# Kernel optimization log

Hardware: AMD Instinct MI355X
Metric: run time of the kernel (lower is better)

Reference implementation:

```python
import jax, jax.numpy as jnp
import numpy as np
from jax import lax

B = 8
SEQ_LEN = 336
PRED_LEN = 336
D_MODEL = 32
D_FF = 64
TOP_K = 3
NUM_KERNELS = 6
WAVELET_SCALE = 4
PERIOD_COEFF = 0.5
T_TOTAL = SEQ_LEN + PRED_LEN
KMAX = 2 * NUM_KERNELS - 1  # 11, largest Inception kernel
N_WAVELET_SCALES = 8


def _int_psi_morlet():
    # pywt integrate_wavelet('morl', precision=10)
    xg = np.linspace(-8.0, 8.0, 1 << 10)
    psi = np.exp(-xg ** 2 / 2.0) * np.cos(5.0 * xg)
    step = xg[1] - xg[0]
    return np.cumsum(psi) * step, xg


def cwt_morl(data, scales):
    # data: (B, N, T) -> coeffs (S, B, N, T); follows pywt/ptwt cwt(..., 'morl')
    int_psi, xg = _int_psi_morlet()
    step = xg[1] - xg[0]
    b, n, t = data.shape
    flat = data.reshape(-1, t)
    outs = []
    for s in scales:
        j = (np.arange(s * (xg[-1] - xg[0]) + 1) / (s * step)).astype(np.int64)
        j = j[j < int_psi.size]
        filt = jnp.asarray(int_psi[j][::-1].copy(), dtype=data.dtype)
        conv = jax.vmap(lambda r: jnp.convolve(r, filt, mode='full'))(flat)
        coef = (-float(np.sqrt(s))) * jnp.diff(conv, axis=-1)
        d = (coef.shape[-1] - t) / 2.0
        coef = coef[:, int(np.floor(d)): coef.shape[-1] - int(np.ceil(d))]
        outs.append(coef.reshape(b, n, t))
    return jnp.stack(outs, 0)


def _conv2d_same(x, w, bias, pad_h, pad_w):
    y = lax.conv_general_dilated(x, w, (1, 1), [(pad_h, pad_h), (pad_w, pad_w)],
                                 dimension_numbers=('NCHW', 'OIHW', 'NCHW'))
    return y + bias[None, :, None, None]


def _inception(x, w, bias):
    # w: (K, O, I, 11, 11) with each k-th kernel (size 2k+1) zero-padded to 11x11.
    # mean of K 'same' convs == one conv with the mean kernel (conv is linear).
    return _conv2d_same(x, w.mean(0), bias.mean(0), KMAX // 2, KMAX // 2)


def _period_conv(x, w1, b1, w2, b2):
    h = jax.nn.gelu(_inception(x, w1, b1), approximate=False)
    return _inception(h, w2, b2)


def _dct2(x):
    # DCT-II over last dim, norm=None (matches torch helper: 2 * Re(W * FFT(perm(x))))
    n = x.shape[-1]
    v = jnp.concatenate([x[..., ::2], x[..., 1::2][..., ::-1]], axis=-1)
    vc = jnp.fft.fft(v, axis=-1)
    k = -jnp.arange(n, dtype=x.dtype) * (np.pi / (2 * n))
    return 2.0 * (vc.real * jnp.cos(k) - vc.imag * jnp.sin(k))


def _dct_block(xcl, ln_w, ln_b, w_fc1, w_fc2):
    # xcl: (B, C, L). Per-channel DCT loop in torch == DCT over last dim.
    f = _dct2(xcl)
    mu = f.mean(-1, keepdims=True)
    var = ((f - mu) ** 2).mean(-1, keepdims=True)
    ln = (f - mu) / jnp.sqrt(var + 1e-6) * ln_w + ln_b
    h = jax.nn.relu(jnp.einsum('bcl,dc->bdl', ln, w_fc1))  # 1x1 conv1d, no bias
    lr = jax.nn.sigmoid(jnp.einsum('bdl,cd->bcl', h, w_fc2))
    return xcl * lr


def _top_periods(x):
    # torch.topk on batch/channel-averaged rfft magnitude; indices are detached
    amp = np.abs(np.fft.rfft(np.asarray(jax.device_get(x)), axis=1))
    freq = amp.mean(axis=(0, 2))
    freq[0] = 0.0
    return np.argsort(-freq)[:TOP_K]


def _forward(x, w_inc1, b_inc1, w_inc2, b_inc2, w_scale, b_scale,
             ln_w, ln_b, w_fc1, w_fc2, w_proj, b_proj, top_list):
    b, t, n = x.shape
    amp = jnp.abs(jnp.fft.rfft(x, axis=1))          # (B, F, N)
    period_weight = amp.mean(-1)[:, top_list]       # (B, k)

    res = []
    for idx in top_list:
        p = t // int(idx)
        length = t if t % p == 0 else (t // p + 1) * p
        out = x if length == t else jnp.concatenate(
            [x, jnp.zeros((b, length - t, n), x.dtype)], axis=1)
        out = out.reshape(b, length // p, p, n).transpose(0, 3, 1, 2)  # (B,N,L/p,p)
        out = _period_conv(out, w_inc1, b_inc1, w_inc2, b_inc2)
        out = out.transpose(0, 2, 3, 1).reshape(b, length, n)[:, :t, :]
        res.append(out)
    res = jnp.stack(res, -1)                         # (B,T,N,k)
    pw = jax.nn.softmax(period_weight, axis=1)       # (B,k)

    scales = 2.0 ** np.linspace(-1, WAVELET_SCALE, N_WAVELET_SCALES)
    coeffs = cwt_morl(x.transpose(0, 2, 1), scales).transpose(1, 2, 0, 3)  # (B,N,8,T)
    wr = _period_conv(coeffs, w_inc1, b_inc1, w_inc2, b_inc2)              # (B,N,8,T)
    # depthwise Conv2d(kernel=(8,1), groups=d_model), squeezes scale axis
    wr = jnp.einsum('bcst,cs->bct', wr, w_scale) + b_scale[None, :, None]  # (B,N,T)
    wr = wr.transpose(0, 2, 1)                       # (B,T,N)

    pc10 = PERIOD_COEFF ** 10
    out = (1.0 - pc10) * wr + pc10 * jnp.einsum('btnk,bk->btn', res, pw)
    out = out + x
    xc = _dct_block(out.transpose(0, 2, 1), ln_w, ln_b, w_fc1, w_fc2)
    out = xc.transpose(0, 2, 1) + x
    y = jnp.einsum('bnt,pt->bnp', out.transpose(0, 2, 1), w_proj) + b_proj
    return y.transpose(0, 2, 1)                      # (B, PRED_LEN, N)


def _masked_inception_weight(key, out_c, in_c):
    w = jax.random.normal(key, (NUM_KERNELS, out_c, in_c, KMAX, KMAX), jnp.float32) * 0.05
    mask = np.zeros((NUM_KERNELS, 1, 1, KMAX, KMAX), np.float32)
    for i in range(NUM_KERNELS):
        ks = 2 * i + 1
        lo = (KMAX - ks) // 2
        mask[i, 0, 0, lo:lo + ks, lo:lo + ks] = 1.0
    return w * jnp.asarray(mask)


def setup_inputs() -> dict:
    key = jax.random.key(0)
    ks = jax.random.split(key, 12)
    return {
        'x': jax.random.normal(ks[0], (B, T_TOTAL, D_MODEL), jnp.float32),
        'w_inc1': _masked_inception_weight(ks[1], D_FF, D_MODEL),
        'b_inc1': jax.random.normal(ks[2], (NUM_KERNELS, D_FF), jnp.float32) * 0.02,
        'w_inc2': _masked_inception_weight(ks[3], D_MODEL, D_FF),
        'b_inc2': jax.random.normal(ks[4], (NUM_KERNELS, D_MODEL), jnp.float32) * 0.02,
        'w_scale': jax.random.normal(ks[5], (D_MODEL, 8), jnp.float32) * 0.1,
        'b_scale': jax.random.normal(ks[6], (D_MODEL,), jnp.float32) * 0.02,
        'ln_w': jnp.ones((T_TOTAL,), jnp.float32),
        'ln_b': jnp.zeros((T_TOTAL,), jnp.float32),
        'w_fc1': jax.random.normal(ks[7], (2 * D_MODEL, D_MODEL), jnp.float32) * 0.1,
        'w_fc2': jax.random.normal(ks[8], (D_MODEL, 2 * D_MODEL), jnp.float32) * 0.1,
        'w_proj': jax.random.normal(ks[9], (PRED_LEN, T_TOTAL), jnp.float32) * 0.02,
        'b_proj': jax.random.normal(ks[10], (PRED_LEN,), jnp.float32) * 0.02,
    }


def reference(x, w_inc1, b_inc1, w_inc2, b_inc2, w_scale, b_scale,
              ln_w, ln_b, w_fc1, w_fc2, w_proj, b_proj):
    top_list = _top_periods(x)  # concrete (detached) indices, like torch
    return _forward(x, w_inc1, b_inc1, w_inc2, b_inc2, w_scale, b_scale,
                    ln_w, ln_b, w_fc1, w_fc2, w_proj, b_proj, top_list)
```

## Files before the change

kernel.cpp:

```cpp
#include <hip/hip_runtime.h>
#include <math.h>

#ifndef M_PI
#define M_PI 3.14159265358979323846
#endif

typedef __attribute__((ext_vector_type(8))) short bf16x8;
typedef __attribute__((ext_vector_type(4))) float f32x4;

struct CwtP {
  double sstep[8];
  float  sqs[8];
  int    L[8];
  int    st0[8];
};

#define OFF_DTABC 0
#define OFF_DTABS 5376
#define OFF_AMP   10752
#define OFF_DCT   32320
#define OFF_DFILT 43072
#define OFF_PW    51520
#define OFF_META  51616
#define OFF_B1    51712
#define OFF_B2    51968
#define OFF_W1T   52224
#define OFF_W2T   547840
#define OFF_XT    1043456
#define OFF_PADW  1731584
#define OFF_PADW2 8016896
#define OFF_WRC2  20587520
#define OFF_POUT2 26092544
#define OFF_OUT1T 30221312
#define OFF_PADP  OFF_PADW
#define OFF_PADP2 OFF_PADW2
#define OFF_LN    26092544
#define OFF_HB    26780672
#define OFF_OUT2T 28156928

__device__ inline unsigned short f2b(float f) {
  unsigned int u = __float_as_uint(f);
  unsigned int r = (u + 0x7fffu + ((u >> 16) & 1u)) >> 16;
  return (unsigned short)r;
}

__global__ void k_tables(double* __restrict__ dtabc, double* __restrict__ dtabs,
                         float* __restrict__ dcttab) {
  int tid = threadIdx.x;
  for (int j = tid; j < 672; j += blockDim.x) {
    double a = (2.0 * M_PI * (double)j) / 672.0;
    dtabc[j] = cos(a);
    dtabs[j] = sin(a);
  }
  for (int j = tid; j < 2688; j += blockDim.x) {
    dcttab[j] = (float)cos(M_PI * (double)j / 1344.0);
  }
}

__global__ void k_wmeanb(const float* __restrict__ w1, const float* __restrict__ b1,
                         const float* __restrict__ w2, const float* __restrict__ b2,
                         unsigned short* __restrict__ W1T, unsigned short* __restrict__ W2T,
                         float* __restrict__ B1, float* __restrict__ B2) {
  int i = blockIdx.x * blockDim.x + threadIdx.x;
  const float inv6 = 1.0f / 6.0f;
  if (i < 247808) {
    float s1 = 0.f, s2 = 0.f;
#pragma unroll
    for (int g = 0; g < 6; ++g) { s1 += w1[g * 247808 + i]; s2 += w2[g * 247808 + i]; }
    s1 *= inv6; s2 *= inv6;
    {
      int co = i / 3872; int r = i - co * 3872;
      int ci = r / 121;  int tap = r - ci * 121;
      W1T[tap * 2048 + co * 32 + ci] = f2b(s1);
    }
    {
      int co = i / 7744; int r = i - co * 7744;
      int ci = r / 121;  int tap = r - ci * 121;
      W2T[tap * 2048 + co * 64 + ci] = f2b(s2);
    }
  } else {
    int j = i - 247808;
    if (j < 64) {
      float s = 0.f;
#pragma unroll
      for (int g = 0; g < 6; ++g) s += b1[g * 64 + j];
      B1[j] = s * inv6;
    } else if (j < 96) {
      int c = j - 64;
      float s = 0.f;
#pragma unroll
      for (int g = 0; g < 6; ++g) s += b2[g * 32 + c];
      B2[c] = s * inv6;
    }
  }
}

__global__ void k_xT(const float* __restrict__ x, float* __restrict__ xT) {
  int i = blockIdx.x * 256 + threadIdx.x;
  if (i >= 8 * 672 * 32) return;
  int n = i & 31;
  int t = (i >> 5) % 672;
  int b = i / (32 * 672);
  xT[(b * 32 + n) * 672 + t] = x[i];
}

__global__ void k_dft(const float* __restrict__ x, const double* __restrict__ tc,
                      const double* __restrict__ ts, double* __restrict__ amp) {
  int k = blockIdx.x, b = blockIdx.y;
  int tid = threadIdx.x;
  int n = tid & 31, half = tid >> 5;
  double re = 0.0, im = 0.0;
  for (int t = half; t < 672; t += 2) {
    double xv = (double)x[(b * 672 + t) * 32 + n];
    int idx = (k * t) % 672;
    re += xv * tc[idx];
    im += xv * ts[idx];
  }
  re += __shfl_xor(re, 32);
  im += __shfl_xor(im, 32);
  double a = sqrt(re * re + im * im);
  for (int off = 16; off >= 1; off >>= 1) a += __shfl_xor(a, off);
  if (tid == 0) amp[b * 337 + k] = a * (1.0 / 32.0);
}

__global__ void k_top(const double* __restrict__ amp, int* __restrict__ meta,
                      float* __restrict__ pw) {
  __shared__ double fr[337];
  __shared__ int sidx[3];
  int tid = threadIdx.x;
  for (int k = tid; k < 337; k += 64) {
    double s = 0.0;
    for (int b = 0; b < 8; ++b) s += amp[b * 337 + k];
    fr[k] = (k == 0) ? -1.0 : s * 0.125;
  }
  __syncthreads();
  if (tid == 0) {
    for (int r = 0; r < 3; ++r) {
      int best = 1; double bv = fr[1];
      for (int k = 2; k < 337; ++k) if (fr[k] > bv) { bv = fr[k]; best = k; }
      fr[best] = -2.0;
      sidx[r] = best;
      meta[r] = best;
      int p = 672 / best;
      meta[3 + r] = p;
      int len = (672 % p == 0) ? 672 : (672 / p + 1) * p;
      meta[6 + r] = len;
      meta[9 + r] = len / p;
    }
  }
  __syncthreads();
  if (tid < 8) {
    int b = tid;
    float v0 = (float)amp[b * 337 + sidx[0]];
    float v1 = (float)amp[b * 337 + sidx[1]];
    float v2 = (float)amp[b * 337 + sidx[2]];
    float m = fmaxf(v0, fmaxf(v1, v2));
    float e0 = expf(v0 - m), e1 = expf(v1 - m), e2 = expf(v2 - m);
    float inv = 1.0f / (e0 + e1 + e2);
    pw[b * 3 + 0] = e0 * inv;
    pw[b * 3 + 1] = e1 * inv;
    pw[b * 3 + 2] = e2 * inv;
  }
}

__global__ void k_dfilt(float* __restrict__ dfilt, CwtP P) {
  __shared__ double ipsi[1024];
  int tid = threadIdx.x;
  const double step = 16.0 / 1023.0;
  double xg = (tid == 1023) ? 8.0 : (-8.0 + (double)tid * step);
  ipsi[tid] = exp(-0.5 * xg * xg) * cos(5.0 * xg);
  __syncthreads();
  for (int off = 1; off < 1024; off <<= 1) {
    double v = ipsi[tid];
    double a = (tid >= off) ? ipsi[tid - off] : 0.0;
    __syncthreads();
    ipsi[tid] = v + a;
    __syncthreads();
  }
  for (int s = 0; s < 8; ++s) {
    int L = P.L[s];
    double sstep = P.sstep[s];
    for (int q = tid; q <= L; q += 1024) {
      float fq = 0.f, fqm = 0.f;
      if (q < L)  { long j = (long)((double)(L - 1 - q) / sstep); fq  = (float)(ipsi[j] * step); }
      if (q >= 1) { long j = (long)((double)(L - q) / sstep);     fqm = (float)(ipsi[j] * step); }
      dfilt[s * 264 + q] = fq - fqm;
    }
  }
}

__global__ void k_cwt(const float* __restrict__ xT, const float* __restrict__ dfilt,
                      unsigned short* __restrict__ PADW, CwtP P) {
  int s = blockIdx.x, n = blockIdx.y, b = blockIdx.z;
  __shared__ float row[672];
  __shared__ float df[264];
  int tid = threadIdx.x;
  int L = P.L[s], st0 = P.st0[s];
  float sq = P.sqs[s];
  for (int i = tid; i < 672; i += blockDim.x) row[i] = xT[(b * 32 + n) * 672 + i];
  for (int i = tid; i <= L; i += blockDim.x) df[i] = dfilt[s * 264 + i];
  __syncthreads();
  for (int t = tid; t < 672; t += blockDim.x) {
    float acc = 0.f;
    int base = t + st0 + 1;
    for (int q = 0; q <= L; ++q) {
      int idx = base - q;
      if (idx >= 0 && idx < 672) acc += df[q] * row[idx];
    }
    PADW[((size_t)(b * 18 + s + 5) * 682 + (t + 5)) * 32 + n] = f2b(-sq * acc);
  }
}

__global__ void k_zero(float4* __restrict__ p, int n16) {
  int i = blockIdx.x * 256 + threadIdx.x;
  int stride = gridDim.x * 256;
  for (; i < n16; i += stride) p[i] = float4{0.f, 0.f, 0.f, 0.f};
}

__global__ void k_pfill(const float* __restrict__ x, unsigned short* __restrict__ PADP,
                        const int* __restrict__ meta, int k) {
  int i = blockIdx.x * 256 + threadIdx.x;
  if (i >= 8 * 672 * 32) return;
  int W = meta[3 + k], H = meta[9 + k];
  int PW = W + 10;
  int ci = i & 31;
  int t = (i >> 5) % 672;
  int b = i / 21504;
  int h = t / W, w = t - h * W;
  PADP[((size_t)(b * (H + 10) + h + 5) * PW + (w + 5)) * 32 + ci] = f2b(x[i]);
}

template <int CIN, int COUT, int MODE>
__global__ __launch_bounds__(256) void k_conv(
    const unsigned short* __restrict__ Pin, const unsigned short* __restrict__ Wt,
    const float* __restrict__ bias, void* __restrict__ outp,
    int Hs, int Ws, int gi, const int* __restrict__ meta, int HWcap, int Tlim) {
  constexpr int NA = COUT / 16;
  constexpr int NS = CIN / 32;
  constexpr int RED = NA * 4 + 1;
  __shared__ float red[4][64][RED];

  int H = Hs, W = Ws;
  if (gi >= 0) { W = meta[3 + gi]; H = meta[9 + gi]; }
  int PW = W + 10;
  int HW = H * W;
  int Tout = (HW < Tlim) ? HW : Tlim;
  int tiles = (Tout + 15) >> 4;
  int total = 8 * tiles;
  int gid = blockIdx.x;
  if (gid >= total) return;
  int q = total >> 3, rr = total & 7;
  int xcd = gid & 7, lid = gid >> 3;
  int wid = (xcd < rr) ? (xcd * (q + 1) + lid)
                       : (rr * (q + 1) + (xcd - rr) * q + lid);
  int ti = wid % tiles; int b = wid / tiles;
  int wv = threadIdx.x >> 6;
  int l = threadIdx.x & 63;
  int lr = l & 15, lk = l >> 4;

  int t = ti * 16 + lr;
  bool valid = (t < Tout);
  unsigned tt = valid ? (unsigned)t : 0u;
  unsigned h = tt / (unsigned)W;
  unsigned w = tt - h * (unsigned)W;

  int h0 = (ti * 16) / W;
  int tl5 = ti * 16 + 15; if (tl5 >= Tout) tl5 = Tout - 1;
  int h1 = tl5 / W;
  int kh_lo = (h1 >= 5) ? 0 : 5 - h1;
  int kh_hi = (H + 4 - h0 < 10) ? (H + 4 - h0) : 10;

  const unsigned short* pB =
      Pin + ((size_t)(b * (H + 10) + h) * PW + w) * CIN + lk * 8;

  f32x4 acc[NA];
#pragma unroll
  for (int c = 0; c < NA; ++c) acc[c] = f32x4{0.f, 0.f, 0.f, 0.f};

  for (int kh = kh_lo + wv; kh <= kh_hi; kh += 4) {
    const unsigned short* pBr = pB + (size_t)kh * PW * CIN;
    const unsigned short* pA =
        Wt + (size_t)(kh * 11) * COUT * CIN + (size_t)lr * CIN + lk * 8;
#pragma unroll
    for (int s = 0; s < NS; ++s) {
      bf16x8 bfr[11];
#pragma unroll
      for (int kw = 0; kw < 11; ++kw)
        bfr[kw] = *(const bf16x8*)(const void*)(pBr + kw * CIN + s * 32);
#pragma unroll
      for (int kw = 0; kw < 11; ++kw) {
#pragma unroll
        for (int c = 0; c < NA; ++c) {
          bf16x8 af = *(const bf16x8*)(const void*)(
              pA + (size_t)kw * COUT * CIN + c * 16 * CIN + s * 32);
          acc[c] = __builtin_amdgcn_mfma_f32_16x16x32_bf16(af, bfr[kw], acc[c], 0, 0, 0);
        }
      }
    }
  }

#pragma unroll
  for (int c = 0; c < NA; ++c)
#pragma unroll
    for (int q2 = 0; q2 < 4; ++q2) red[wv][l][c * 4 + q2] = acc[c][q2];
  __syncthreads();

  if (wv >= NA || !valid) return;
  int c = wv;
  int co0 = c * 16 + lk * 4;
  float v[4];
#pragma unroll
  for (int q2 = 0; q2 < 4; ++q2) {
    float s = red[0][l][c * 4 + q2] + red[1][l][c * 4 + q2] +
              red[2][l][c * 4 + q2] + red[3][l][c * 4 + q2];
    s += bias[co0 + q2];
    if (MODE == 0) s = 0.5f * s * (1.0f + erff(s * 0.70710678118654752f));
    v[q2] = s;
  }
  if (MODE == 0) {
    unsigned short* Po = (unsigned short*)outp;
    size_t oa = ((size_t)(b * (H + 10) + h + 5) * PW + (w + 5)) * COUT + co0;
    uint2 pk;
    pk.x = (unsigned int)f2b(v[0]) | ((unsigned int)f2b(v[1]) << 16);
    pk.y = (unsigned int)f2b(v[2]) | ((unsigned int)f2b(v[3]) << 16);
    *(uint2*)(void*)(Po + oa) = pk;
  } else {
    float* Fo = (float*)outp;
    size_t oa = ((size_t)b * HWcap + t) * COUT + co0;
    f32x4 vv = {v[0], v[1], v[2], v[3]};
    *(f32x4*)(void*)(Fo + oa) = vv;
  }
}

__global__ void k_combine(const float* __restrict__ WRC2, const float* __restrict__ w_scale,
                          const float* __restrict__ b_scale, const float* __restrict__ POUT2,
                          const float* __restrict__ pw, const float* __restrict__ xT,
                          float* __restrict__ out1T) {
  int b = blockIdx.y;
  int tid = threadIdx.x;
  int n = tid & 31;
  int t = blockIdx.x * 8 + (tid >> 5);
  float wv = b_scale[n];
#pragma unroll
  for (int s = 0; s < 8; ++s)
    wv += WRC2[((size_t)(b * 5376 + s * 672 + t)) * 32 + n] * w_scale[n * 8 + s];
  float p0 = pw[b * 3 + 0], p1 = pw[b * 3 + 1], p2 = pw[b * 3 + 2];
  size_t bi = (size_t)(b * 1344 + t) * 32 + n;
  float rs = p0 * POUT2[bi] + p1 * POUT2[344064 + bi] + p2 * POUT2[688128 + bi];
  const float pc10 = 1.0f / 1024.0f;
  out1T[(b * 32 + n) * 672 + t] =
      (1.0f - pc10) * wv + pc10 * rs + xT[(b * 32 + n) * 672 + t];
}

__global__ void k_dct_ln(const float* __restrict__ out1T, const float* __restrict__ dcttab,
                         const float* __restrict__ ln_w, const float* __restrict__ ln_b,
                         float* __restrict__ ln) {
  int c = blockIdx.x, b = blockIdx.y;
  __shared__ float row[672];
  __shared__ float tab[2688];
  __shared__ float s1[4], s2[4];
  int tid = threadIdx.x;
  for (int i = tid; i < 672; i += 256) row[i] = out1T[(b * 32 + c) * 672 + i];
  for (int i = tid; i < 2688; i += 256) tab[i] = dcttab[i];
  __syncthreads();
  float fv[3];
  float sum = 0.f, sumsq = 0.f;
#pragma unroll
  for (int r = 0; r < 3; ++r) {
    int k = tid + r * 256;
    float acc = 0.f;
    if (k < 672) {
      int idx = k;
      int stp = (2 * k) % 2688;
      for (int m = 0; m < 672; ++m) {
        acc += row[m] * tab[idx];
        idx += stp;
        if (idx >= 2688) idx -= 2688;
      }
      acc *= 2.0f;
      sum += acc;
      sumsq += acc * acc;
    }
    fv[r] = acc;
  }
  for (int off = 32; off >= 1; off >>= 1) {
    sum += __shfl_xor(sum, off);
    sumsq += __shfl_xor(sumsq, off);
  }
  if ((tid & 63) == 0) { s1[tid >> 6] = sum; s2[tid >> 6] = sumsq; }
  __syncthreads();
  float tsum = s1[0] + s1[1] + s1[2] + s1[3];
  float tsq = s2[0] + s2[1] + s2[2] + s2[3];
  float mu = tsum * (1.0f / 672.0f);
  float var = tsq * (1.0f / 672.0f) - mu * mu;
  float rstd = rsqrtf(var + 1e-6f);
#pragma unroll
  for (int r = 0; r < 3; ++r) {
    int k = tid + r * 256;
    if (k < 672)
      ln[(b * 32 + c) * 672 + k] = (fv[r] - mu) * rstd * ln_w[k] + ln_b[k];
  }
}

__global__ void k_fc1(const float* __restrict__ ln, const float* __restrict__ w_fc1,
                      float* __restrict__ h) {
  int d = blockIdx.x, b = blockIdx.y;
  int tid = threadIdx.x;
  __shared__ float wv[32];
  if (tid < 32) wv[tid] = w_fc1[d * 32 + tid];
  __syncthreads();
  for (int t = tid; t < 672; t += 256) {
    float s = 0.f;
#pragma unroll
    for (int c = 0; c < 32; ++c) s += ln[(b * 32 + c) * 672 + t] * wv[c];
    h[(b * 64 + d) * 672 + t] = fmaxf(s, 0.f);
  }
}

__global__ void k_fc2o(const float* __restrict__ h, const float* __restrict__ w_fc2,
                       const float* __restrict__ out1T, const float* __restrict__ xT,
                       float* __restrict__ out2T) {
  int c = blockIdx.x, b = blockIdx.y;
  int tid = threadIdx.x;
  __shared__ float wv[64];
  if (tid < 64) wv[tid] = w_fc2[c * 64 + tid];
  __syncthreads();
  for (int t = tid; t < 672; t += 256) {
    float s = 0.f;
#pragma unroll
    for (int d = 0; d < 64; ++d) s += h[(b * 64 + d) * 672 + t] * wv[d];
    float lr = 1.0f / (1.0f + expf(-s));
    out2T[(b * 32 + c) * 672 + t] =
        out1T[(b * 32 + c) * 672 + t] * lr + xT[(b * 32 + c) * 672 + t];
  }
}

__global__ void k_proj(const float* __restrict__ out2T, const float* __restrict__ w_proj,
                       const float* __restrict__ b_proj, float* __restrict__ out) {
  int p = blockIdx.x, b = blockIdx.y;
  int tid = threadIdx.x;
  int n = tid & 31, half = tid >> 5;
  float acc = 0.f;
  for (int t = half; t < 672; t += 2)
    acc += out2T[(b * 32 + n) * 672 + t] * w_proj[p * 672 + t];
  acc += __shfl_xor(acc, 32);
  if (tid < 32) out[(b * 336 + p) * 32 + n] = acc + b_proj[p];
}

extern "C" void kernel_launch(void* const* d_in, const int* in_sizes, int n_in,
                              void* d_out, int out_size, void* d_ws, size_t ws_size,
                              hipStream_t stream) {
  (void)in_sizes; (void)n_in; (void)out_size; (void)ws_size;
  const float* x      = (const float*)d_in[0];
  const float* w_inc1 = (const float*)d_in[1];
  const float* b_inc1 = (const float*)d_in[2];
  const float* w_inc2 = (const float*)d_in[3];
  const float* b_inc2 = (const float*)d_in[4];
  const float* w_scale= (const float*)d_in[5];
  const float* b_scale= (const float*)d_in[6];
  const float* ln_w   = (const float*)d_in[7];
  const float* ln_b   = (const float*)d_in[8];
  const float* w_fc1  = (const float*)d_in[9];
  const float* w_fc2  = (const float*)d_in[10];
  const float* w_proj = (const float*)d_in[11];
  const float* b_proj = (const float*)d_in[12];
  float* out = (float*)d_out;

  char* ws = (char*)d_ws;
  double* dtabc = (double*)(ws + OFF_DTABC);
  double* dtabs = (double*)(ws + OFF_DTABS);
  double* amp   = (double*)(ws + OFF_AMP);
  float* dcttab = (float*)(ws + OFF_DCT);
  float* dfilt  = (float*)(ws + OFF_DFILT);
  float* pw     = (float*)(ws + OFF_PW);
  int*   meta   = (int*)(ws + OFF_META);
  float* B1     = (float*)(ws + OFF_B1);
  float* B2     = (float*)(ws + OFF_B2);
  unsigned short* W1T = (unsigned short*)(ws + OFF_W1T);
  unsigned short* W2T = (unsigned short*)(ws + OFF_W2T);
  float* xT     = (float*)(ws + OFF_XT);
  unsigned short* PADW  = (unsigned short*)(ws + OFF_PADW);
  unsigned short* PADW2 = (unsigned short*)(ws + OFF_PADW2);
  unsigned short* PADP  = (unsigned short*)(ws + OFF_PADP);
  unsigned short* PADP2 = (unsigned short*)(ws + OFF_PADP2);
  float* WRC2  = (float*)(ws + OFF_WRC2);
  float* POUT2 = (float*)(ws + OFF_POUT2);
  float* out1T = (float*)(ws + OFF_OUT1T);
  float* lnb   = (float*)(ws + OFF_LN);
  float* hb    = (float*)(ws + OFF_HB);
  float* out2T = (float*)(ws + OFF_OUT2T);

  CwtP P;
  const double step = 16.0 / 1023.0;
  for (int i = 0; i < 8; ++i) {
    double e = (i == 7) ? 4.0 : (-1.0 + (double)i * (5.0 / 7.0));
    double s = pow(2.0, e);
    double sstep = s * step;
    int Na = (int)ceil(16.0 * s + 1.0);
    int L = 0;
    for (int k = 0; k < Na; ++k) {
      long j = (long)((double)k / sstep);
      if (j < 1024) L++;
      else break;
    }
    P.sstep[i] = sstep;
    P.L[i] = L;
    P.st0[i] = (L - 2) / 2;
    P.sqs[i] = (float)sqrt(s);
  }

  k_tables<<<1, 256, 0, stream>>>(dtabc, dtabs, dcttab);
  k_wmeanb<<<(247808 + 96 + 255) / 256, 256, 0, stream>>>(w_inc1, b_inc1, w_inc2, b_inc2,
                                                          W1T, W2T, B1, B2);
  k_xT<<<672, 256, 0, stream>>>(x, xT);
  k_dfilt<<<1, 1024, 0, stream>>>(dfilt, P);
  k_dft<<<dim3(337, 8), 64, 0, stream>>>(x, dtabc, dtabs, amp);
  k_top<<<1, 64, 0, stream>>>(amp, meta, pw);

  k_zero<<<2048, 256, 0, stream>>>((float4*)(ws + OFF_PADW), 1178496);
  k_cwt<<<dim3(8, 32, 8), 256, 0, stream>>>(xT, dfilt, PADW, P);
  k_conv<32, 64, 0><<<2688, 256, 0, stream>>>(PADW, W1T, B1, (void*)PADW2,
                                              8, 672, -1, meta, 0, 1 << 30);
  k_conv<64, 32, 1><<<2688, 256, 0, stream>>>(PADW2, W2T, B2, (void*)WRC2,
                                              8, 672, -1, meta, 5376, 1 << 30);

  for (int k = 0; k < 3; ++k) {
    k_zero<<<1024, 256, 0, stream>>>((float4*)(ws + OFF_PADP), 240064);
    k_zero<<<2048, 256, 0, stream>>>((float4*)(ws + OFF_PADP2), 480128);
    k_pfill<<<672, 256, 0, stream>>>(x, PADP, meta, k);
    k_conv<32, 64, 0><<<672, 256, 0, stream>>>(PADP, W1T, B1, (void*)PADP2,
                                               0, 0, k, meta, 0, 1 << 30);
    k_conv<64, 32, 1><<<336, 256, 0, stream>>>(PADP2, W2T, B2,
                                               (void*)(POUT2 + (size_t)k * 344064),
                                               0, 0, k, meta, 1344, 672);
  }

  k_combine<<<dim3(84, 8), 256, 0, stream>>>(WRC2, w_scale, b_scale, POUT2, pw, xT, out1T);
  k_dct_ln<<<dim3(32, 8), 256, 0, stream>>>(out1T, dcttab, ln_w, ln_b, lnb);
  k_fc1<<<dim3(64, 8), 256, 0, stream>>>(lnb, w_fc1, hb);
  k_fc2o<<<dim3(32, 8), 256, 0, stream>>>(hb, w_fc2, out1T, xT, out2T);
  k_proj<<<dim3(336, 8), 64, 0, stream>>>(out2T, w_proj, b_proj, out);
}
```

Baseline: 967.2 us.

## Split conv work across waves by output-channel block instead of kernel rows

The MFMA conv kernel previously split the 11 kernel rows across 4 waves and reduced partial accumulators through shared memory with a block barrier. Now each wave owns one 16-channel output block, and for COUT=32 two spatial tiles per block, looping over all kernel rows itself. This removes the LDS reduction and __syncthreads and halves the grid for the second conv. In exchange each wave does a longer serial loop, each position's input fragments are reloaded once per channel block, and there is less parallelism across kernel rows.

```diff
diff --git a/kernel.cpp b/kernel.cpp
--- a/kernel.cpp
+++ b/kernel.cpp
@@ -235,10 +235,9 @@
     const unsigned short* __restrict__ Pin, const unsigned short* __restrict__ Wt,
     const float* __restrict__ bias, void* __restrict__ outp,
     int Hs, int Ws, int gi, const int* __restrict__ meta, int HWcap, int Tlim) {
-  constexpr int NA = COUT / 16;
+  constexpr int NCO = COUT / 16;
+  constexpr int TPB = 4 / NCO;
   constexpr int NS = CIN / 32;
-  constexpr int RED = NA * 4 + 1;
-  __shared__ float red[4][64][RED];
 
   int H = Hs, W = Ws;
   if (gi >= 0) { W = meta[3 + gi]; H = meta[9 + gi]; }
@@ -246,17 +245,22 @@
   int HW = H * W;
   int Tout = (HW < Tlim) ? HW : Tlim;
   int tiles = (Tout + 15) >> 4;
-  int total = 8 * tiles;
+  int tgroups = (tiles + TPB - 1) / TPB;
+  int total = 8 * tgroups;
   int gid = blockIdx.x;
   if (gid >= total) return;
   int q = total >> 3, rr = total & 7;
   int xcd = gid & 7, lid = gid >> 3;
   int wid = (xcd < rr) ? (xcd * (q + 1) + lid)
                        : (rr * (q + 1) + (xcd - rr) * q + lid);
-  int ti = wid % tiles; int b = wid / tiles;
+  int tg = wid % tgroups; int b = wid / tgroups;
   int wv = threadIdx.x >> 6;
   int l = threadIdx.x & 63;
   int lr = l & 15, lk = l >> 4;
+
+  int ti = tg * TPB + wv / NCO;
+  int c  = wv % NCO;
+  if (ti >= tiles) return;
 
   int t = ti * 16 + lr;
   bool valid = (t < Tout);
@@ -272,48 +276,34 @@
 
   const unsigned short* pB =
       Pin + ((size_t)(b * (H + 10) + h) * PW + w) * CIN + lk * 8;
-
-  f32x4 acc[NA];
-#pragma unroll
-  for (int c = 0; c < NA; ++c) acc[c] = f32x4{0.f, 0.f, 0.f, 0.f};
-
-  for (int kh = kh_lo + wv; kh <= kh_hi; kh += 4) {
+  const unsigned short* pAc =
+      Wt + (size_t)c * 16 * CIN + (size_t)lr * CIN + lk * 8;
+
+  f32x4 acc = f32x4{0.f, 0.f, 0.f, 0.f};
+
+  for (int kh = kh_lo; kh <= kh_hi; ++kh) {
     const unsigned short* pBr = pB + (size_t)kh * PW * CIN;
-    const unsigned short* pA =
-        Wt + (size_t)(kh * 11) * COUT * CIN + (size_t)lr * CIN + lk * 8;
+    const unsigned short* pA = pAc + (size_t)(kh * 11) * COUT * CIN;
 #pragma unroll
     for (int s = 0; s < NS; ++s) {
-      bf16x8 bfr[11];
+      bf16x8 bfr[11], afr[11];
+#pragma unroll
+      for (int kw = 0; kw < 11; ++kw) {
+        bfr[kw] = *(const bf16x8*)(const void*)(pBr + kw * CIN + s * 32);
+        afr[kw] = *(const bf16x8*)(const void*)(pA + (size_t)kw * COUT * CIN + s * 32);
+      }
 #pragma unroll
       for (int kw = 0; kw < 11; ++kw)
-        bfr[kw] = *(const bf16x8*)(const void*)(pBr + kw * CIN + s * 32);
-#pragma unroll
-      for (int kw = 0; kw < 11; ++kw) {
-#pragma unroll
-        for (int c = 0; c < NA; ++c) {
-          bf16x8 af = *(const bf16x8*)(const void*)(
-              pA + (size_t)kw * COUT * CIN + c * 16 * CIN + s * 32);
-          acc[c] = __builtin_amdgcn_mfma_f32_16x16x32_bf16(af, bfr[kw], acc[c], 0, 0, 0);
-        }
-      }
-    }
-  }
-
-#pragma unroll
-  for (int c = 0; c < NA; ++c)
-#pragma unroll
-    for (int q2 = 0; q2 < 4; ++q2) red[wv][l][c * 4 + q2] = acc[c][q2];
-  __syncthreads();
-
-  if (wv >= NA || !valid) return;
-  int c = wv;
+        acc = __builtin_amdgcn_mfma_f32_16x16x32_bf16(afr[kw], bfr[kw], acc, 0, 0, 0);
+    }
+  }
+
+  if (!valid) return;
   int co0 = c * 16 + lk * 4;
   float v[4];
 #pragma unroll
   for (int q2 = 0; q2 < 4; ++q2) {
-    float s = red[0][l][c * 4 + q2] + red[1][l][c * 4 + q2] +
-              red[2][l][c * 4 + q2] + red[3][l][c * 4 + q2];
-    s += bias[co0 + q2];
+    float s = acc[q2] + bias[co0 + q2];
     if (MODE == 0) s = 0.5f * s * (1.0f + erff(s * 0.70710678118654752f));
     v[q2] = s;
   }
@@ -521,7 +511,7 @@
   k_cwt<<<dim3(8, 32, 8), 256, 0, stream>>>(xT, dfilt, PADW, P);
   k_conv<32, 64, 0><<<2688, 256, 0, stream>>>(PADW, W1T, B1, (void*)PADW2,
                                               8, 672, -1, meta, 0, 1 << 30);
-  k_conv<64, 32, 1><<<2688, 256, 0, stream>>>(PADW2, W2T, B2, (void*)WRC2,
+  k_conv<64, 32, 1><<<1344, 256, 0, stream>>>(PADW2, W2T, B2, (void*)WRC2,
                                               8, 672, -1, meta, 5376, 1 << 30);
 
   for (int k = 0; k < 3; ++k) {
@@ -530,7 +520,7 @@
     k_pfill<<<672, 256, 0, stream>>>(x, PADP, meta, k);
     k_conv<32, 64, 0><<<672, 256, 0, stream>>>(PADP, W1T, B1, (void*)PADP2,
                                                0, 0, k, meta, 0, 1 << 30);
-    k_conv<64, 32, 1><<<336, 256, 0, stream>>>(PADP2, W2T, B2,
+    k_conv<64, 32, 1><<<168, 256, 0, stream>>>(PADP2, W2T, B2,
                                                (void*)(POUT2 + (size_t)k * 344064),
                                                0, 0, k, meta, 1344, 672);
   }
```

Measured after the change: 1.118 ms. 15.6% more time.

## Process two spatial tiles per block in wavelet convs to reuse weight fragments

Applied to the files above, without the earlier changes.

Templates the MFMA conv kernel on NB, the number of 16-pixel tiles each block handles. With NB=2 for the large wavelet-branch convolutions, each loaded weight fragment feeds two MFMAs, and the grid is halved. This roughly halves weight-load traffic per output but doubles the accumulators and input fragments held in registers. It also adds a waves-per-EU hint, which may cause register pressure or spills.

```diff
diff --git a/kernel.cpp b/kernel.cpp
--- a/kernel.cpp
+++ b/kernel.cpp
@@ -230,14 +230,15 @@
   PADP[((size_t)(b * (H + 10) + h + 5) * PW + (w + 5)) * 32 + ci] = f2b(x[i]);
 }
 
-template <int CIN, int COUT, int MODE>
-__global__ __launch_bounds__(256) void k_conv(
+template <int CIN, int COUT, int MODE, int NB>
+__global__ __launch_bounds__(256) __attribute__((amdgpu_waves_per_eu(2, 4)))
+void k_conv(
     const unsigned short* __restrict__ Pin, const unsigned short* __restrict__ Wt,
     const float* __restrict__ bias, void* __restrict__ outp,
     int Hs, int Ws, int gi, const int* __restrict__ meta, int HWcap, int Tlim) {
   constexpr int NA = COUT / 16;
   constexpr int NS = CIN / 32;
-  constexpr int RED = NA * 4 + 1;
+  constexpr int RED = NB * NA * 4 + 1;
   __shared__ float red[4][64][RED];
 
   int H = Hs, W = Ws;
@@ -246,54 +247,68 @@
   int HW = H * W;
   int Tout = (HW < Tlim) ? HW : Tlim;
   int tiles = (Tout + 15) >> 4;
-  int total = 8 * tiles;
+  int tgroups = (tiles + NB - 1) / NB;
+  int total = 8 * tgroups;
   int gid = blockIdx.x;
   if (gid >= total) return;
   int q = total >> 3, rr = total & 7;
   int xcd = gid & 7, lid = gid >> 3;
   int wid = (xcd < rr) ? (xcd * (q + 1) + lid)
                        : (rr * (q + 1) + (xcd - rr) * q + lid);
-  int ti = wid % tiles; int b = wid / tiles;
+  int tg = wid % tgroups; int b = wid / tgroups;
   int wv = threadIdx.x >> 6;
   int l = threadIdx.x & 63;
   int lr = l & 15, lk = l >> 4;
-
-  int t = ti * 16 + lr;
-  bool valid = (t < Tout);
-  unsigned tt = valid ? (unsigned)t : 0u;
-  unsigned h = tt / (unsigned)W;
-  unsigned w = tt - h * (unsigned)W;
-
-  int h0 = (ti * 16) / W;
-  int tl5 = ti * 16 + 15; if (tl5 >= Tout) tl5 = Tout - 1;
-  int h1 = tl5 / W;
+  int ti0 = tg * NB;
+
+  bool val[NB];
+  unsigned hj[NB], wj[NB];
+  const unsigned short* pB[NB];
+#pragma unroll
+  for (int j = 0; j < NB; ++j) {
+    int t = (ti0 + j) * 16 + lr;
+    bool v = (t < Tout);
+    val[j] = v;
+    unsigned tt = v ? (unsigned)t : 0u;
+    hj[j] = tt / (unsigned)W;
+    wj[j] = tt - hj[j] * (unsigned)W;
+    pB[j] = Pin + ((size_t)(b * (H + 10) + hj[j]) * PW + wj[j]) * CIN + lk * 8;
+  }
+
+  int h0 = (ti0 * 16) / W;
+  int tlast = (ti0 + NB) * 16 - 1; if (tlast >= Tout) tlast = Tout - 1;
+  int h1 = tlast / W;
   int kh_lo = (h1 >= 5) ? 0 : 5 - h1;
   int kh_hi = (H + 4 - h0 < 10) ? (H + 4 - h0) : 10;
 
-  const unsigned short* pB =
-      Pin + ((size_t)(b * (H + 10) + h) * PW + w) * CIN + lk * 8;
-
-  f32x4 acc[NA];
-#pragma unroll
-  for (int c = 0; c < NA; ++c) acc[c] = f32x4{0.f, 0.f, 0.f, 0.f};
+  f32x4 acc[NA][NB];
+#pragma unroll
+  for (int c = 0; c < NA; ++c)
+#pragma unroll
+    for (int j = 0; j < NB; ++j) acc[c][j] = f32x4{0.f, 0.f, 0.f, 0.f};
 
   for (int kh = kh_lo + wv; kh <= kh_hi; kh += 4) {
-    const unsigned short* pBr = pB + (size_t)kh * PW * CIN;
     const unsigned short* pA =
         Wt + (size_t)(kh * 11) * COUT * CIN + (size_t)lr * CIN + lk * 8;
 #pragma unroll
     for (int s = 0; s < NS; ++s) {
-      bf16x8 bfr[11];
-#pragma unroll
-      for (int kw = 0; kw < 11; ++kw)
-        bfr[kw] = *(const bf16x8*)(const void*)(pBr + kw * CIN + s * 32);
+      bf16x8 bfr[NB][11];
+#pragma unroll
+      for (int j = 0; j < NB; ++j)
+#pragma unroll
+        for (int kw = 0; kw < 11; ++kw)
+          bfr[j][kw] = *(const bf16x8*)(const void*)(
+              pB[j] + (size_t)kh * PW * CIN + kw * CIN + s * 32);
 #pragma unroll
       for (int kw = 0; kw < 11; ++kw) {
 #pragma unroll
         for (int c = 0; c < NA; ++c) {
           bf16x8 af = *(const bf16x8*)(const void*)(
               pA + (size_t)kw * COUT * CIN + c * 16 * CIN + s * 32);
-          acc[c] = __builtin_amdgcn_mfma_f32_16x16x32_bf16(af, bfr[kw], acc[c], 0, 0, 0);
+#pragma unroll
+          for (int j = 0; j < NB; ++j)
+            acc[c][j] = __builtin_amdgcn_mfma_f32_16x16x32_bf16(af, bfr[j][kw],
+                                                                acc[c][j], 0, 0, 0);
         }
       }
     }
@@ -302,33 +317,41 @@
 #pragma unroll
   for (int c = 0; c < NA; ++c)
 #pragma unroll
-    for (int q2 = 0; q2 < 4; ++q2) red[wv][l][c * 4 + q2] = acc[c][q2];
-  __syncthreads();
-
-  if (wv >= NA || !valid) return;
+    for (int j = 0; j < NB; ++j)
+#pragma unroll
+      for (int q2 = 0; q2 < 4; ++q2)
+        red[wv][l][(c * NB + j) * 4 + q2] = acc[c][j][q2];
+  __syncthreads();
+
+  if (wv >= NA) return;
   int c = wv;
   int co0 = c * 16 + lk * 4;
-  float v[4];
-#pragma unroll
-  for (int q2 = 0; q2 < 4; ++q2) {
-    float s = red[0][l][c * 4 + q2] + red[1][l][c * 4 + q2] +
-              red[2][l][c * 4 + q2] + red[3][l][c * 4 + q2];
-    s += bias[co0 + q2];
-    if (MODE == 0) s = 0.5f * s * (1.0f + erff(s * 0.70710678118654752f));
-    v[q2] = s;
-  }
-  if (MODE == 0) {
-    unsigned short* Po = (unsigned short*)outp;
-    size_t oa = ((size_t)(b * (H + 10) + h + 5) * PW + (w + 5)) * COUT + co0;
-    uint2 pk;
-    pk.x = (unsigned int)f2b(v[0]) | ((unsigned int)f2b(v[1]) << 16);
-    pk.y = (unsigned int)f2b(v[2]) | ((unsigned int)f2b(v[3]) << 16);
-    *(uint2*)(void*)(Po + oa) = pk;
-  } else {
-    float* Fo = (float*)outp;
-    size_t oa = ((size_t)b * HWcap + t) * COUT + co0;
-    f32x4 vv = {v[0], v[1], v[2], v[3]};
-    *(f32x4*)(void*)(Fo + oa) = vv;
+#pragma unroll
+  for (int j = 0; j < NB; ++j) {
+    if (!val[j]) continue;
+    int t = (ti0 + j) * 16 + lr;
+    float v[4];
+#pragma unroll
+    for (int q2 = 0; q2 < 4; ++q2) {
+      float s = red[0][l][(c * NB + j) * 4 + q2] + red[1][l][(c * NB + j) * 4 + q2] +
+                red[2][l][(c * NB + j) * 4 + q2] + red[3][l][(c * NB + j) * 4 + q2];
+      s += bias[co0 + q2];
+      if (MODE == 0) s = 0.5f * s * (1.0f + erff(s * 0.70710678118654752f));
+      v[q2] = s;
+    }
+    if (MODE == 0) {
+      unsigned short* Po = (unsigned short*)outp;
+      size_t oa = ((size_t)(b * (H + 10) + hj[j] + 5) * PW + (wj[j] + 5)) * COUT + co0;
+      uint2 pk;
+      pk.x = (unsigned int)f2b(v[0]) | ((unsigned int)f2b(v[1]) << 16);
+      pk.y = (unsigned int)f2b(v[2]) | ((unsigned int)f2b(v[3]) << 16);
+      *(uint2*)(void*)(Po + oa) = pk;
+    } else {
+      float* Fo = (float*)outp;
+      size_t oa = ((size_t)b * HWcap + t) * COUT + co0;
+      f32x4 vv = {v[0], v[1], v[2], v[3]};
+      *(f32x4*)(void*)(Fo + oa) = vv;
+    }
   }
 }
 
@@ -519,20 +542,20 @@
 
   k_zero<<<2048, 256, 0, stream>>>((float4*)(ws + OFF_PADW), 1178496);
   k_cwt<<<dim3(8, 32, 8), 256, 0, stream>>>(xT, dfilt, PADW, P);
-  k_conv<32, 64, 0><<<2688, 256, 0, stream>>>(PADW, W1T, B1, (void*)PADW2,
-                                              8, 672, -1, meta, 0, 1 << 30);
-  k_conv<64, 32, 1><<<2688, 256, 0, stream>>>(PADW2, W2T, B2, (void*)WRC2,
-                                              8, 672, -1, meta, 5376, 1 << 30);
+  k_conv<32, 64, 0, 2><<<1344, 256, 0, stream>>>(PADW, W1T, B1, (void*)PADW2,
+                                                 8, 672, -1, meta, 0, 1 << 30);
+  k_conv<64, 32, 1, 2><<<1344, 256, 0, stream>>>(PADW2, W2T, B2, (void*)WRC2,
+                                                 8, 672, -1, meta, 5376, 1 << 30);
 
   for (int k = 0; k < 3; ++k) {
     k_zero<<<1024, 256, 0, stream>>>((float4*)(ws + OFF_PADP), 240064);
     k_zero<<<2048, 256, 0, stream>>>((float4*)(ws + OFF_PADP2), 480128);
     k_pfill<<<672, 256, 0, stream>>>(x, PADP, meta, k);
-    k_conv<32, 64, 0><<<672, 256, 0, stream>>>(PADP, W1T, B1, (void*)PADP2,
-                                               0, 0, k, meta, 0, 1 << 30);
-    k_conv<64, 32, 1><<<336, 256, 0, stream>>>(PADP2, W2T, B2,
-                                               (void*)(POUT2 + (size_t)k * 344064),
-                                               0, 0, k, meta, 1344, 672);
+    k_conv<32, 64, 0, 1><<<672, 256, 0, stream>>>(PADP, W1T, B1, (void*)PADP2,
+                                                  0, 0, k, meta, 0, 1 << 30);
+    k_conv<64, 32, 1, 1><<<336, 256, 0, stream>>>(PADP2, W2T, B2,
+                                                  (void*)(POUT2 + (size_t)k * 344064),
+                                                  0, 0, k, meta, 1344, 672);
   }
 
   k_combine<<<dim3(84, 8), 256, 0, stream>>>(WRC2, w_scale, b_scale, POUT2, pw, xT, out1T);
```

After: 910.5 us. 5.9% less time.
